# Performance work log

Measured on AMD Instinct MI355X. Metric: run time of the kernel, lower is better.

## Reference

```python
import jax, jax.numpy as jnp
import numpy as np

D = 1024      # embedding_dim
FW = 64       # filter_width
DEPTH = 2     # recurrence_depth
E = D * (DEPTH + 1)  # expanded dim = 3072
B, L = 2, 4096


def setup_inputs() -> dict:
    key = jax.random.key(0)
    ks = jax.random.split(key, 12)
    s = lambda k, shape, scale: jax.random.normal(k, shape, dtype=jnp.float32) * scale
    return {
        "x": jax.random.normal(ks[0], (B, L, D), dtype=jnp.float32),
        # input_projection: Linear(D, E)  (stored as [in,out])
        "w_in": s(ks[1], (D, E), 0.02), "b_in": jnp.zeros((E,), jnp.float32),
        # depthwise Conv1d(E, E, k=3, padding=2, groups=E): torch weight [E,1,3]
        "w_conv": s(ks[2], (E, 1, 3), 0.5), "b_conv": jnp.zeros((E,), jnp.float32),
        # HyenaFilter MLP: Linear(3,FW) -> SiLU -> Linear(FW,FW) -> SiLU -> Linear(FW, D, bias=False)
        "w1": s(ks[3], (3, FW), 0.5), "b1": jnp.zeros((FW,), jnp.float32),
        "w2": s(ks[4], (FW, FW), 0.1), "b2": jnp.zeros((FW,), jnp.float32),
        "w3": s(ks[5], (FW, D), 0.1),
        # HyenaFilter.bias parameter (output_channels = D*(DEPTH-1) = D)
        "filt_bias": jax.random.normal(ks[6], (D,), dtype=jnp.float32),
        # output_projection: Linear(D, D)
        "w_out": s(ks[7], (D, D), 0.02), "b_out": jnp.zeros((D,), jnp.float32),
    }


def _fftconv(x_bdl, h, bias_d):
    Lq = x_bdl.shape[-1]
    n = 2 * Lq
    Xf = jnp.fft.rfft(x_bdl, n=n)                       # [b,d,n//2+1]
    Hf = jnp.fft.rfft(h, n=n) / n                       # broadcast over [b,d]
    y = jnp.fft.irfft(Xf * Hf, n=n, norm="forward")[..., :Lq]
    return y + x_bdl * bias_d[:, None]


def reference(x, w_in, b_in, w_conv, b_conv, w1, b1, w2, b2, w3, filt_bias, w_out, b_out):
    _, Lx, Dm = x.shape
    # expand_input: Linear then b l e -> b e l
    u = (x @ w_in + b_in).transpose(0, 2, 1)            # [B,E,L]
    # depthwise short conv, padding=2 then truncate to L (causal-ish, as in source)
    u = jax.lax.conv_general_dilated(
        u, w_conv, window_strides=(1,), padding=[(2, 2)],
        feature_group_count=u.shape[1], dimension_numbers=("NCH", "OIH", "NCH"))
    u = (u + b_conv[None, :, None])[..., :Lx]
    streams = [u[:, i * Dm:(i + 1) * Dm, :] for i in range(DEPTH + 1)]  # each [B,D,L]
    # implicit filter generation
    t = jnp.linspace(0.0, 1.0, Lx)                       # [L]
    pos = jnp.tile(t[:, None], (1, 3))                   # [L,3]
    hmlp = jax.nn.silu(pos @ w1 + b1)
    hmlp = jax.nn.silu(hmlp @ w2 + b2)
    filters = (hmlp @ w3) * jnp.exp(-t[:, None] * jnp.abs(filt_bias)[None, :])  # [L,D]
    # recurrence (depth=2 -> single gated long conv); source indexes filters by ROW i
    v = streams[-1]
    for i in range(DEPTH - 1):
        v = v * streams[i]
        v = _fftconv(v, filters[i], filt_bias)
    # merge with stream 0, back to [B,L,D], output projection
    out = (v * streams[0]).transpose(0, 2, 1) @ w_out + b_out
    return out
```

## Files before the change

kernel.cpp:

```cpp
#include <hip/hip_runtime.h>
#include <hip/hip_bf16.h>


typedef __bf16 bf16x8 __attribute__((ext_vector_type(8)));
typedef float  f32x4  __attribute__((ext_vector_type(4)));

typedef const __attribute__((address_space(1))) unsigned int GU32;
typedef __attribute__((address_space(3))) unsigned int LU32;
#define GLL16(gp, lp) __builtin_amdgcn_global_load_lds((GU32*)(gp), (LU32*)(lp), 16, 0, 0)

#define CFENCE asm volatile("" ::: "memory")
#define SBAR   do { CFENCE; __builtin_amdgcn_s_barrier(); CFENCE; } while (0)
#define SCHEDB __builtin_amdgcn_sched_barrier(0)
#define VMCNT8 asm volatile("s_waitcnt vmcnt(8)" ::: "memory")
#define VMCNT0 asm volatile("s_waitcnt vmcnt(0)" ::: "memory")

__device__ __forceinline__ float silu(float x) { return x / (1.f + __expf(-x)); }

__global__ __launch_bounds__(256) void hgen(const float* __restrict__ b1,
                                            const float* __restrict__ w2,
                                            const float* __restrict__ b2,
                                            const float* __restrict__ w3,
                                            float* __restrict__ h) {
    __shared__ float hm2[64];
    int t = threadIdx.x;
    if (t < 64) {
        float acc = b2[t];
        for (int f = 0; f < 64; ++f) acc += silu(b1[f]) * w2[f * 64 + t];
        hm2[t] = silu(acc);
    }
    __syncthreads();
    for (int r = 0; r < 4; ++r) {
        int j = t * 4 + r;
        float acc = 0.f;
        for (int g = 0; g < 64; ++g) acc += hm2[g] * w3[g * 1024 + j];
        h[j] = acc;
    }
}

__global__ void hfrag(const float* __restrict__ h, __bf16* __restrict__ af) {
    int sp = blockIdx.x;
    int lane = threadIdx.x;
    int m = lane & 15, kh = lane >> 4;
    bf16x8 v;
    #pragma unroll
    for (int j = 0; j < 8; ++j) {
        int k = kh * 8 + j;
        int idx = (k < 16) ? (32 * sp + m - k) : (32 * sp + 32 + m - k);
        float val = (idx >= 0 && idx < 1024) ? h[idx] : 0.f;
        v[j] = (__bf16)val;
    }
    *(bf16x8*)&af[(size_t)(sp * 64 + lane) * 8] = v;
}

__global__ __launch_bounds__(256) void cvt_x(const float* __restrict__ x,
                                             __bf16* __restrict__ xb) {
    size_t i = ((size_t)blockIdx.x * 256 + threadIdx.x) * 8;
    f32x4 a = *(const f32x4*)&x[i];
    f32x4 b = *(const f32x4*)&x[i + 4];
    bf16x8 v;
    v[0] = (__bf16)a[0]; v[1] = (__bf16)a[1]; v[2] = (__bf16)a[2]; v[3] = (__bf16)a[3];
    v[4] = (__bf16)b[0]; v[5] = (__bf16)b[1]; v[6] = (__bf16)b[2]; v[7] = (__bf16)b[3];
    *(bf16x8*)&xb[i] = v;
}

__global__ __launch_bounds__(256) void tcvt(const float* __restrict__ src,
                                            __bf16* __restrict__ dst,
                                            int ld, int cbase) {
    __shared__ __bf16 tile[64][65];
    int t = threadIdx.x;
    int k0 = blockIdx.x * 64, n0 = blockIdx.y * 64;
    int c = t & 63, rg = t >> 6;
    #pragma unroll
    for (int i = 0; i < 16; ++i) {
        int r = rg * 16 + i;
        tile[r][c] = (__bf16)src[(size_t)(k0 + r) * ld + cbase + n0 + c];
    }
    __syncthreads();
    #pragma unroll
    for (int i = 0; i < 16; ++i) {
        int nn = rg * 16 + i;
        dst[(size_t)(n0 + nn) * 1024 + k0 + c] = tile[c][nn];
    }
}

__device__ __forceinline__ void stage_half(const __bf16* __restrict__ panel, int kk,
                                           char* ldshalf, int t) {
    int c1 = t, c2 = t + 512;
    int s1 = c1 ^ ((c1 >> 3) & 7);
    int s2 = c2 ^ ((c2 >> 3) & 7);
    GLL16(panel + (size_t)(s1 >> 3) * 1024 + kk + (s1 & 7) * 8, ldshalf + c1 * 16);
    GLL16(panel + (size_t)(s2 >> 3) * 1024 + kk + (s2 & 7) * 8, ldshalf + c2 * 16);
}

__global__ __launch_bounds__(512, 1) void gemm256(const __bf16* __restrict__ A,
                                                  const __bf16* __restrict__ Bt,
                                                  const float* __restrict__ bias,
                                                  __bf16* __restrict__ out0,
                                                  __bf16* __restrict__ out1) {
    __shared__ __bf16 lds[65536];
    char* L = (char*)lds;
    int t = threadIdx.x, lane = t & 63, w = t >> 6;
    int wr = w >> 2, wc = w & 3;
    int m0 = blockIdx.x * 256, n0 = blockIdx.y * 256;
    int rl = lane & 15, kh8 = (lane >> 4) * 8;
    int nloc = (wc & 1) * 64;

    const __bf16* pa0 = A + (size_t)m0 * 1024;
    const __bf16* pa1 = A + (size_t)(m0 + 128) * 1024;
    const __bf16* pb0 = Bt + (size_t)n0 * 1024;
    const __bf16* pb1 = Bt + (size_t)(n0 + 128) * 1024;

    f32x4 acc[8][4] = {};
    bf16x8 ar[4][2], br[4][2];

#define RDA(dst, mf, ks) do { int _a = bA + ((mf) * 16 + rl) * 128 + ((ks) * 32 + kh8) * 2; \
        _a ^= (_a >> 3) & 0x70; dst = *(const bf16x8*)(L + _a); } while (0)
#define RDB(dst, nf, ks) do { int _a = bB + (nloc + (nf) * 16 + rl) * 128 + ((ks) * 32 + kh8) * 2; \
        _a ^= (_a >> 3) & 0x70; dst = *(const bf16x8*)(L + _a); } while (0)

    stage_half(pb0, 0, L + 65536, t);
    stage_half(pb1, 0, L + 65536 + 16384, t);
    stage_half(pa0, 0, L, t);
    stage_half(pa1, 0, L + 16384, t);
    stage_half(pb0, 64, L + 65536 + 32768, t);
    stage_half(pb1, 64, L + 65536 + 32768 + 16384, t);
    stage_half(pa0, 64, L + 32768, t);
    stage_half(pa1, 64, L + 32768 + 16384, t);
    VMCNT8;
    SBAR;

    for (int kt = 0; kt < 16; ++kt) {
        int p = kt & 1;
        int bA = p * 32768 + wr * 16384;
        int bB = 65536 + p * 32768 + (wc >> 1) * 16384;
        int kk2 = (kt + 2) * 64;
        char* LA = L + p * 32768;
        char* LB = L + 65536 + p * 32768;

        #pragma unroll
        for (int i = 0; i < 4; ++i) { RDA(ar[i][0], i, 0); RDA(ar[i][1], i, 1); }
        RDB(br[0][0], 0, 0); RDB(br[0][1], 0, 1);
        RDB(br[1][0], 1, 0); RDB(br[1][1], 1, 1);
        SCHEDB; SBAR; SCHEDB;
        __builtin_amdgcn_s_setprio(1);
        #pragma unroll
        for (int mf = 0; mf < 4; ++mf)
            #pragma unroll
            for (int nf = 0; nf < 2; ++nf)
                #pragma unroll
                for (int ks = 0; ks < 2; ++ks)
                    acc[mf][nf] = __builtin_amdgcn_mfma_f32_16x16x32_bf16(ar[mf][ks], br[nf][ks], acc[mf][nf], 0, 0, 0);
        __builtin_amdgcn_s_setprio(0);
        SCHEDB; SBAR; SCHEDB;

        RDB(br[2][0], 2, 0); RDB(br[2][1], 2, 1);
        RDB(br[3][0], 3, 0); RDB(br[3][1], 3, 1);
        SCHEDB; SBAR; SCHEDB;
        __builtin_amdgcn_s_setprio(1);
        #pragma unroll
        for (int mf = 0; mf < 4; ++mf)
            #pragma unroll
            for (int nf = 2; nf < 4; ++nf)
                #pragma unroll
                for (int ks = 0; ks < 2; ++ks)
                    acc[mf][nf] = __builtin_amdgcn_mfma_f32_16x16x32_bf16(ar[mf][ks], br[nf][ks], acc[mf][nf], 0, 0, 0);
        __builtin_amdgcn_s_setprio(0);
        SCHEDB; SBAR; SCHEDB;

        #pragma unroll
        for (int i = 0; i < 4; ++i) { RDA(ar[i][0], 4 + i, 0); RDA(ar[i][1], 4 + i, 1); }
        if (kt < 14) {
            stage_half(pb0, kk2, LB, t);
            stage_half(pb1, kk2, LB + 16384, t);
        }
        SCHEDB; SBAR; SCHEDB;
        __builtin_amdgcn_s_setprio(1);
        #pragma unroll
        for (int mf = 0; mf < 4; ++mf)
            #pragma unroll
            for (int nf = 0; nf < 2; ++nf)
                #pragma unroll
                for (int ks = 0; ks < 2; ++ks)
                    acc[4 + mf][nf] = __builtin_amdgcn_mfma_f32_16x16x32_bf16(ar[mf][ks], br[nf][ks], acc[4 + mf][nf], 0, 0, 0);
        __builtin_amdgcn_s_setprio(0);
        SCHEDB; SBAR; SCHEDB;

        if (kt < 14) {
            stage_half(pa0, kk2, LA, t);
            stage_half(pa1, kk2, LA + 16384, t);
        }
        SCHEDB; SBAR; SCHEDB;
        __builtin_amdgcn_s_setprio(1);
        #pragma unroll
        for (int mf = 0; mf < 4; ++mf)
            #pragma unroll
            for (int nf = 2; nf < 4; ++nf)
                #pragma unroll
                for (int ks = 0; ks < 2; ++ks)
                    acc[4 + mf][nf] = __builtin_amdgcn_mfma_f32_16x16x32_bf16(ar[mf][ks], br[nf][ks], acc[4 + mf][nf], 0, 0, 0);
        __builtin_amdgcn_s_setprio(0);
        if (kt < 14)      { VMCNT8; }
        else if (kt == 14){ VMCNT0; }
        SCHEDB; SBAR; SCHEDB;
    }
#undef RDA
#undef RDB

    int cb = lane & 15, rb = (lane >> 4) * 4;
    #pragma unroll
    for (int nf = 0; nf < 4; ++nf) {
        int col = n0 + wc * 64 + nf * 16 + cb;
        __bf16* uo = (col < 1024) ? out0 : out1;
        int oc = col & 1023;
        float bv = bias[(col < 1024) ? col : 1024 + col];
        #pragma unroll
        for (int mf = 0; mf < 8; ++mf) {
            int row = m0 + wr * 128 + mf * 16 + rb;
            #pragma unroll
            for (int j = 0; j < 4; ++j)
                uo[(size_t)(row + j) * 1024 + oc] = (__bf16)(acc[mf][nf][j] + bv);
        }
    }
}

template<int EPI>
__global__ __launch_bounds__(256) void gemm128(const __bf16* __restrict__ A,
                                               const __bf16* __restrict__ Bt,
                                               const float* __restrict__ bias,
                                               void* __restrict__ out0,
                                               void* __restrict__ out1) {
    __shared__ __bf16 As[128 * 32];
    __shared__ __bf16 Bs[128 * 32];
    int t = threadIdx.x, lane = t & 63, w = t >> 6;
    int m0 = blockIdx.x * 128, n0 = blockIdx.y * 128;
    int wr = (w >> 1) * 64, wc = (w & 1) * 64;
    f32x4 acc[4][4] = {};

    int s1 = w * 64 + lane;
    int s2 = s1 + 256;
    const __bf16* a1 = A + (size_t)(m0 + (s1 >> 2)) * 1024 + (s1 & 3) * 8;
    const __bf16* a2 = A + (size_t)(m0 + (s2 >> 2)) * 1024 + (s2 & 3) * 8;
    const __bf16* b1 = Bt + (size_t)(n0 + (s1 >> 2)) * 1024 + (s1 & 3) * 8;
    const __bf16* b2 = Bt + (size_t)(n0 + (s2 >> 2)) * 1024 + (s2 & 3) * 8;

    for (int kk = 0; kk < 1024; kk += 32) {
        GLL16(a1 + kk, (char*)&As[(size_t)s1 * 8]);
        GLL16(a2 + kk, (char*)&As[(size_t)s2 * 8]);
        GLL16(b1 + kk, (char*)&Bs[(size_t)s1 * 8]);
        GLL16(b2 + kk, (char*)&Bs[(size_t)s2 * 8]);
        __syncthreads();
        int kh = (lane >> 4) * 8, rl = lane & 15;
        bf16x8 af[4], bf[4];
        #pragma unroll
        for (int i = 0; i < 4; ++i) {
            af[i] = *(const bf16x8*)&As[(wr + i * 16 + rl) * 32 + kh];
            bf[i] = *(const bf16x8*)&Bs[(wc + i * 16 + rl) * 32 + kh];
        }
        #pragma unroll
        for (int mi = 0; mi < 4; ++mi)
            #pragma unroll
            for (int ni = 0; ni < 4; ++ni)
                acc[mi][ni] = __builtin_amdgcn_mfma_f32_16x16x32_bf16(af[mi], bf[ni], acc[mi][ni], 0, 0, 0);
        __syncthreads();
    }

    int cb = lane & 15, rb = (lane >> 4) * 4;
    #pragma unroll
    for (int ni = 0; ni < 4; ++ni) {
        int col = n0 + wc + ni * 16 + cb;
        if (EPI == 0) {
            __bf16* uo = (col < 1024) ? (__bf16*)out0 : (__bf16*)out1;
            int oc = col & 1023;
            float bv = bias[(col < 1024) ? col : 1024 + col];
            #pragma unroll
            for (int mi = 0; mi < 4; ++mi) {
                int row = m0 + wr + mi * 16 + rb;
                #pragma unroll
                for (int j = 0; j < 4; ++j)
                    uo[(size_t)(row + j) * 1024 + oc] = (__bf16)(acc[mi][ni][j] + bv);
            }
        } else {
            float* o = (float*)out0;
            float bv = bias[col];
            #pragma unroll
            for (int mi = 0; mi < 4; ++mi) {
                int row = m0 + wr + mi * 16 + rb;
                #pragma unroll
                for (int j = 0; j < 4; ++j)
                    o[(size_t)(row + j) * 1024 + col] = acc[mi][ni][j] + bv;
            }
        }
    }
}

__global__ __launch_bounds__(256) void convmul(const __bf16* __restrict__ u0,
                                               const __bf16* __restrict__ u2,
                                               const float* __restrict__ w_conv,
                                               const float* __restrict__ b_conv,
                                               __bf16* __restrict__ v,
                                               __bf16* __restrict__ st) {
    __shared__ float vt[64][65];
    int t = threadIdx.x;
    int b = blockIdx.z;
    int l0b = blockIdx.x * 64;
    int d0 = blockIdx.y * 64;
    int d = t & 63, lg = t >> 6;
    int col = d0 + d;
    int l0 = l0b + lg * 16;

    float c00 = w_conv[col * 3 + 0], c01 = w_conv[col * 3 + 1], c02 = w_conv[col * 3 + 2];
    float bc0 = b_conv[col];
    int e2 = 2048 + col;
    float c20 = w_conv[e2 * 3 + 0], c21 = w_conv[e2 * 3 + 1], c22 = w_conv[e2 * 3 + 2];
    float bc2 = b_conv[e2];

    size_t base = ((size_t)b * 4096 + l0) * 1024 + col;
    float p01 = (l0 >= 1) ? (float)u0[base - 1024] : 0.f;
    float p02 = (l0 >= 2) ? (float)u0[base - 2048] : 0.f;
    float p21 = (l0 >= 1) ? (float)u2[base - 1024] : 0.f;
    float p22 = (l0 >= 2) ? (float)u2[base - 2048] : 0.f;
    #pragma unroll
    for (int il = 0; il < 16; ++il) {
        float c0v = (float)u0[base + (size_t)il * 1024];
        float c2v = (float)u2[base + (size_t)il * 1024];
        float s0v = c00 * p02 + c01 * p01 + c02 * c0v + bc0;
        float s2v = c20 * p22 + c21 * p21 + c22 * c2v + bc2;
        p02 = p01; p01 = c0v; p22 = p21; p21 = c2v;
        vt[lg * 16 + il][d] = s0v * s2v;
        st[base + (size_t)il * 1024] = (__bf16)s0v;
    }
    __syncthreads();
    int lo = t & 63, dg = t >> 6;
    size_t obase = ((size_t)b * 1024 + d0 + dg * 16) * 4096 + l0b + lo;
    #pragma unroll
    for (int id = 0; id < 16; ++id)
        v[obase + (size_t)id * 4096] = (__bf16)vt[lo][dg * 16 + id];
}

__global__ __launch_bounds__(256) void firk(const __bf16* __restrict__ v,
                                            const __bf16* __restrict__ afg,
                                            const float* __restrict__ filt_bias,
                                            __bf16* __restrict__ z) {
    __shared__ __bf16 vlds[768 * 8];
    __shared__ __bf16 alds[33 * 64 * 8];
    int t = threadIdx.x;
    int bd = blockIdx.x;
    int d = bd & 1023;
    const __bf16* vrow = v + (size_t)bd * 4096;

    for (int c = t; c < 33 * 64; c += 256)
        *(bf16x8*)&alds[c * 8] = *(const bf16x8*)&afg[(size_t)c * 8];
    #pragma unroll
    for (int i = 0; i < 3; ++i) {
        int c = t + i * 256;
        bf16x8 val = {};
        if (c >= 130 && c < 642) val = *(const bf16x8*)&vrow[(c - 130) * 8];
        int cs = c ^ ((c >> 3) & 7);
        *(bf16x8*)&vlds[cs * 8] = val;
    }
    __syncthreads();

    int lane = t & 63, w = t >> 6;
    int n = lane & 15, kh = lane >> 4;
    int khoff = (kh == 0) ? 0 : (kh == 1) ? 8 : (kh == 2) ? -16 : -8;
    f32x4 acc[4] = {};
    for (int sp = 0; sp < 33; ++sp) {
        bf16x8 af = *(const bf16x8*)&alds[(sp * 64 + lane) * 8];
        #pragma unroll
        for (int ct = 0; ct < 4; ++ct) {
            int p = w * 64 + ct * 16 + n;
            int e = 16 * p - 32 * sp + 1040 + khoff;
            int c = e >> 3;
            int cs = c ^ ((c >> 3) & 7);
            bf16x8 bfv = *(const bf16x8*)&vlds[cs * 8];
            acc[ct] = __builtin_amdgcn_mfma_f32_16x16x32_bf16(af, bfv, acc[ct], 0, 0, 0);
        }
    }

    float fb = filt_bias[d];
    __bf16* zrow = z + (size_t)bd * 4096;
    #pragma unroll
    for (int ct = 0; ct < 4; ++ct) {
        int p = w * 64 + ct * 16 + n;
        #pragma unroll
        for (int j = 0; j < 4; ++j) {
            int l = 16 * p + kh * 4 + j;
            int e = l + 1040;
            int c = e >> 3;
            int cs = c ^ ((c >> 3) & 7);
            float vv = (float)vlds[cs * 8 + (e & 7)];
            zrow[l] = (__bf16)(acc[ct][j] + vv * fb);
        }
    }
}

__global__ __launch_bounds__(256) void trz(const __bf16* __restrict__ zz,
                                           const __bf16* __restrict__ st,
                                           __bf16* __restrict__ zt) {
    __shared__ __bf16 tile[64][65];
    int t = threadIdx.x;
    int l0 = blockIdx.x * 64, d0 = blockIdx.y * 64, b = blockIdx.z;
    int c = t & 63, rg = t >> 6;
    #pragma unroll
    for (int i = 0; i < 16; ++i) {
        int r = rg * 16 + i;
        tile[r][c] = zz[((size_t)(b * 1024 + d0 + r)) * 4096 + l0 + c];
    }
    __syncthreads();
    #pragma unroll
    for (int i = 0; i < 16; ++i) {
        int li = rg * 16 + i;
        size_t o = ((size_t)b * 4096 + l0 + li) * 1024 + d0 + c;
        zt[o] = (__bf16)((float)tile[c][li] * (float)st[o]);
    }
}

extern "C" void kernel_launch(void* const* d_in, const int* in_sizes, int n_in,
                              void* d_out, int out_size, void* d_ws, size_t ws_size,
                              hipStream_t stream) {
    const float* x      = (const float*)d_in[0];
    const float* w_in   = (const float*)d_in[1];
    const float* b_in   = (const float*)d_in[2];
    const float* w_conv = (const float*)d_in[3];
    const float* b_conv = (const float*)d_in[4];
    const float* b1     = (const float*)d_in[6];
    const float* w2     = (const float*)d_in[7];
    const float* b2     = (const float*)d_in[8];
    const float* w3     = (const float*)d_in[9];
    const float* fb     = (const float*)d_in[10];
    const float* w_out  = (const float*)d_in[11];
    const float* b_out  = (const float*)d_in[12];
    float* out = (float*)d_out;

    char* ws = (char*)d_ws;
    float*  h  = (float*)ws;
    __bf16* af = (__bf16*)(ws + 4096);
    const size_t SEG = (size_t)8192 * 1024;
    __bf16* X  = (__bf16*)(ws + 40960);
    __bf16* U0 = X + SEG;
    __bf16* U2 = U0 + SEG;
    __bf16* ST = U2 + SEG;
    __bf16* WT = ST + SEG - (size_t)2048 * 1024;

    hgen<<<1, 256, 0, stream>>>(b1, w2, b2, w3, h);
    hfrag<<<33, 64, 0, stream>>>(h, af);
    cvt_x<<<4096, 256, 0, stream>>>(x, X);
    tcvt<<<dim3(16, 16), 256, 0, stream>>>(w_in, WT, 3072, 0);
    tcvt<<<dim3(16, 16), 256, 0, stream>>>(w_in, WT + (size_t)1024 * 1024, 3072, 2048);
    gemm256<<<dim3(32, 8), 512, 0, stream>>>(X, WT, b_in, U0, U2);
    convmul<<<dim3(64, 16, 2), 256, 0, stream>>>(U0, U2, w_conv, b_conv, X, ST);
    firk<<<2048, 256, 0, stream>>>(X, af, fb, U2);
    tcvt<<<dim3(16, 16), 256, 0, stream>>>(w_out, X, 1024, 0);
    trz<<<dim3(64, 16, 2), 256, 0, stream>>>(U2, ST, U0);
    gemm128<1><<<dim3(64, 8), 256, 0, stream>>>(U0, X, b_out, (void*)out, nullptr);
}
```

Measured before the change: 270.9 us.

## Fuse filter fragment build into hgen, drop sched barriers, reorder GEMM epilogues

Merges the hfrag kernel into hgen so the filter is built in shared memory and packed into MFMA fragments within one launch, removing one launch and a global round trip. It also removes the sched_barrier and compiler memory fences around the s_barriers in the main 256-tile GEMM, letting the compiler reorder LDS reads and MFMAs across them. The GEMM epilogues are restructured to hoist bias loads and output pointer selection and to iterate row-major, and gemm128 loses its template parameter. Dropping the fences risks the compiler moving LDS accesses across barriers or changing the intended interleaving.

```diff
diff --git a/kernel.cpp b/kernel.cpp
--- a/kernel.cpp
+++ b/kernel.cpp
@@ -9,9 +9,7 @@
 typedef __attribute__((address_space(3))) unsigned int LU32;
 #define GLL16(gp, lp) __builtin_amdgcn_global_load_lds((GU32*)(gp), (LU32*)(lp), 16, 0, 0)
 
-#define CFENCE asm volatile("" ::: "memory")
-#define SBAR   do { CFENCE; __builtin_amdgcn_s_barrier(); CFENCE; } while (0)
-#define SCHEDB __builtin_amdgcn_sched_barrier(0)
+#define SBAR   __builtin_amdgcn_s_barrier()
 #define VMCNT8 asm volatile("s_waitcnt vmcnt(8)" ::: "memory")
 #define VMCNT0 asm volatile("s_waitcnt vmcnt(0)" ::: "memory")
 
@@ -21,8 +19,9 @@
                                             const float* __restrict__ w2,
                                             const float* __restrict__ b2,
                                             const float* __restrict__ w3,
-                                            float* __restrict__ h) {
+                                            __bf16* __restrict__ af) {
     __shared__ float hm2[64];
+    __shared__ float hl[1024];
     int t = threadIdx.x;
     if (t < 64) {
         float acc = b2[t];
@@ -34,23 +33,22 @@
         int j = t * 4 + r;
         float acc = 0.f;
         for (int g = 0; g < 64; ++g) acc += hm2[g] * w3[g * 1024 + j];
-        h[j] = acc;
-    }
-}
-
-__global__ void hfrag(const float* __restrict__ h, __bf16* __restrict__ af) {
-    int sp = blockIdx.x;
-    int lane = threadIdx.x;
-    int m = lane & 15, kh = lane >> 4;
-    bf16x8 v;
-    #pragma unroll
-    for (int j = 0; j < 8; ++j) {
-        int k = kh * 8 + j;
-        int idx = (k < 16) ? (32 * sp + m - k) : (32 * sp + 32 + m - k);
-        float val = (idx >= 0 && idx < 1024) ? h[idx] : 0.f;
-        v[j] = (__bf16)val;
-    }
-    *(bf16x8*)&af[(size_t)(sp * 64 + lane) * 8] = v;
+        hl[j] = acc;
+    }
+    __syncthreads();
+    for (int c = t; c < 33 * 64; c += 256) {
+        int sp = c >> 6, lane = c & 63;
+        int m = lane & 15, kh = lane >> 4;
+        bf16x8 v;
+        #pragma unroll
+        for (int j = 0; j < 8; ++j) {
+            int k = kh * 8 + j;
+            int idx = (k < 16) ? (32 * sp + m - k) : (32 * sp + 32 + m - k);
+            float val = (idx >= 0 && idx < 1024) ? hl[idx] : 0.f;
+            v[j] = (__bf16)val;
+        }
+        *(bf16x8*)&af[(size_t)c * 8] = v;
+    }
 }
 
 __global__ __launch_bounds__(256) void cvt_x(const float* __restrict__ x,
@@ -142,7 +140,7 @@
         for (int i = 0; i < 4; ++i) { RDA(ar[i][0], i, 0); RDA(ar[i][1], i, 1); }
         RDB(br[0][0], 0, 0); RDB(br[0][1], 0, 1);
         RDB(br[1][0], 1, 0); RDB(br[1][1], 1, 1);
-        SCHEDB; SBAR; SCHEDB;
+        SBAR;
         __builtin_amdgcn_s_setprio(1);
         #pragma unroll
         for (int mf = 0; mf < 4; ++mf)
@@ -152,11 +150,11 @@
                 for (int ks = 0; ks < 2; ++ks)
                     acc[mf][nf] = __builtin_amdgcn_mfma_f32_16x16x32_bf16(ar[mf][ks], br[nf][ks], acc[mf][nf], 0, 0, 0);
         __builtin_amdgcn_s_setprio(0);
-        SCHEDB; SBAR; SCHEDB;
+        SBAR;
 
         RDB(br[2][0], 2, 0); RDB(br[2][1], 2, 1);
         RDB(br[3][0], 3, 0); RDB(br[3][1], 3, 1);
-        SCHEDB; SBAR; SCHEDB;
+        SBAR;
         __builtin_amdgcn_s_setprio(1);
         #pragma unroll
         for (int mf = 0; mf < 4; ++mf)
@@ -166,7 +164,7 @@
                 for (int ks = 0; ks < 2; ++ks)
                     acc[mf][nf] = __builtin_amdgcn_mfma_f32_16x16x32_bf16(ar[mf][ks], br[nf][ks], acc[mf][nf], 0, 0, 0);
         __builtin_amdgcn_s_setprio(0);
-        SCHEDB; SBAR; SCHEDB;
+        SBAR;
 
         #pragma unroll
         for (int i = 0; i < 4; ++i) { RDA(ar[i][0], 4 + i, 0); RDA(ar[i][1], 4 + i, 1); }
@@ -174,7 +172,7 @@
             stage_half(pb0, kk2, LB, t);
             stage_half(pb1, kk2, LB + 16384, t);
         }
-        SCHEDB; SBAR; SCHEDB;
+        SBAR;
         __builtin_amdgcn_s_setprio(1);
         #pragma unroll
         for (int mf = 0; mf < 4; ++mf)
@@ -184,13 +182,13 @@
                 for (int ks = 0; ks < 2; ++ks)
                     acc[4 + mf][nf] = __builtin_amdgcn_mfma_f32_16x16x32_bf16(ar[mf][ks], br[nf][ks], acc[4 + mf][nf], 0, 0, 0);
         __builtin_amdgcn_s_setprio(0);
-        SCHEDB; SBAR; SCHEDB;
+        SBAR;
 
         if (kt < 14) {
             stage_half(pa0, kk2, LA, t);
             stage_half(pa1, kk2, LA + 16384, t);
         }
-        SCHEDB; SBAR; SCHEDB;
+        SBAR;
         __builtin_amdgcn_s_setprio(1);
         #pragma unroll
         for (int mf = 0; mf < 4; ++mf)
@@ -202,34 +200,35 @@
         __builtin_amdgcn_s_setprio(0);
         if (kt < 14)      { VMCNT8; }
         else if (kt == 14){ VMCNT0; }
-        SCHEDB; SBAR; SCHEDB;
+        SBAR;
     }
 #undef RDA
 #undef RDB
 
     int cb = lane & 15, rb = (lane >> 4) * 4;
+    int colb = n0 + wc * 64 + cb;
+    __bf16* uo = (colb < 1024) ? out0 : out1;
+    float bv[4];
     #pragma unroll
     for (int nf = 0; nf < 4; ++nf) {
-        int col = n0 + wc * 64 + nf * 16 + cb;
-        __bf16* uo = (col < 1024) ? out0 : out1;
-        int oc = col & 1023;
-        float bv = bias[(col < 1024) ? col : 1024 + col];
-        #pragma unroll
-        for (int mf = 0; mf < 8; ++mf) {
-            int row = m0 + wr * 128 + mf * 16 + rb;
-            #pragma unroll
-            for (int j = 0; j < 4; ++j)
-                uo[(size_t)(row + j) * 1024 + oc] = (__bf16)(acc[mf][nf][j] + bv);
-        }
-    }
-}
-
-template<int EPI>
+        int col = colb + nf * 16;
+        bv[nf] = bias[(col < 1024) ? col : 1024 + col];
+    }
+    #pragma unroll
+    for (int mf = 0; mf < 8; ++mf)
+        #pragma unroll
+        for (int j = 0; j < 4; ++j) {
+            size_t base = (size_t)(m0 + wr * 128 + mf * 16 + rb + j) * 1024;
+            #pragma unroll
+            for (int nf = 0; nf < 4; ++nf)
+                uo[base + ((colb + nf * 16) & 1023)] = (__bf16)(acc[mf][nf][j] + bv[nf]);
+        }
+}
+
 __global__ __launch_bounds__(256) void gemm128(const __bf16* __restrict__ A,
                                                const __bf16* __restrict__ Bt,
                                                const float* __restrict__ bias,
-                                               void* __restrict__ out0,
-                                               void* __restrict__ out1) {
+                                               float* __restrict__ out) {
     __shared__ __bf16 As[128 * 32];
     __shared__ __bf16 Bs[128 * 32];
     int t = threadIdx.x, lane = t & 63, w = t >> 6;
@@ -266,32 +265,18 @@
     }
 
     int cb = lane & 15, rb = (lane >> 4) * 4;
-    #pragma unroll
-    for (int ni = 0; ni < 4; ++ni) {
-        int col = n0 + wc + ni * 16 + cb;
-        if (EPI == 0) {
-            __bf16* uo = (col < 1024) ? (__bf16*)out0 : (__bf16*)out1;
-            int oc = col & 1023;
-            float bv = bias[(col < 1024) ? col : 1024 + col];
-            #pragma unroll
-            for (int mi = 0; mi < 4; ++mi) {
-                int row = m0 + wr + mi * 16 + rb;
-                #pragma unroll
-                for (int j = 0; j < 4; ++j)
-                    uo[(size_t)(row + j) * 1024 + oc] = (__bf16)(acc[mi][ni][j] + bv);
-            }
-        } else {
-            float* o = (float*)out0;
-            float bv = bias[col];
-            #pragma unroll
-            for (int mi = 0; mi < 4; ++mi) {
-                int row = m0 + wr + mi * 16 + rb;
-                #pragma unroll
-                for (int j = 0; j < 4; ++j)
-                    o[(size_t)(row + j) * 1024 + col] = acc[mi][ni][j] + bv;
-            }
-        }
-    }
+    float bv[4];
+    #pragma unroll
+    for (int ni = 0; ni < 4; ++ni) bv[ni] = bias[n0 + wc + ni * 16 + cb];
+    #pragma unroll
+    for (int mi = 0; mi < 4; ++mi)
+        #pragma unroll
+        for (int j = 0; j < 4; ++j) {
+            size_t base = (size_t)(m0 + wr + mi * 16 + rb + j) * 1024 + n0 + wc + cb;
+            #pragma unroll
+            for (int ni = 0; ni < 4; ++ni)
+                out[base + ni * 16] = acc[mi][ni][j] + bv[ni];
+        }
 }
 
 __global__ __launch_bounds__(256) void convmul(const __bf16* __restrict__ u0,
@@ -434,7 +419,6 @@
     float* out = (float*)d_out;
 
     char* ws = (char*)d_ws;
-    float*  h  = (float*)ws;
     __bf16* af = (__bf16*)(ws + 4096);
     const size_t SEG = (size_t)8192 * 1024;
     __bf16* X  = (__bf16*)(ws + 40960);
@@ -443,8 +427,7 @@
     __bf16* ST = U2 + SEG;
     __bf16* WT = ST + SEG - (size_t)2048 * 1024;
 
-    hgen<<<1, 256, 0, stream>>>(b1, w2, b2, w3, h);
-    hfrag<<<33, 64, 0, stream>>>(h, af);
+    hgen<<<1, 256, 0, stream>>>(b1, w2, b2, w3, af);
     cvt_x<<<4096, 256, 0, stream>>>(x, X);
     tcvt<<<dim3(16, 16), 256, 0, stream>>>(w_in, WT, 3072, 0);
     tcvt<<<dim3(16, 16), 256, 0, stream>>>(w_in, WT + (size_t)1024 * 1024, 3072, 2048);
@@ -453,5 +436,5 @@
     firk<<<2048, 256, 0, stream>>>(X, af, fb, U2);
     tcvt<<<dim3(16, 16), 256, 0, stream>>>(w_out, X, 1024, 0);
     trz<<<dim3(64, 16, 2), 256, 0, stream>>>(U2, ST, U0);
-    gemm128<1><<<dim3(64, 8), 256, 0, stream>>>(U0, X, b_out, (void*)out, nullptr);
-}
+    gemm128<<<dim3(64, 8), 256, 0, stream>>>(U0, X, b_out, out);
+}
```

After: 242.9 us. -10.3%, faster.
